# Kernel tuning notes

Measured on AMD Instinct MI355X. Metric: run time of the kernel, lower is better.

The kernel has to match this reference:

```python
import jax, jax.numpy as jnp
import numpy as np

B, H, S, D = 2, 16, 2048, 64


def setup_inputs() -> dict:
    key = jax.random.key(0)
    k1, k2, k3, k4 = jax.random.split(key, 4)
    Hin = jax.random.normal(k1, (B, H, S, D), dtype=jnp.float32)
    Hk = jax.random.normal(k2, (B, H, S, D), dtype=jnp.float32)
    Hv = jax.random.normal(k3, (B, H, S, D), dtype=jnp.float32)
    # causal lookahead mask: 1 above diagonal (disallowed), 0 elsewhere
    mask = jnp.triu(jnp.ones((S, S), dtype=jnp.float32), k=1)[None, None, :, :]
    # per-head learned G_LM cache matrix avAp: [H, D, D]
    avAp = jax.random.normal(k4, (H, D, D), dtype=jnp.float32) * (1.0 / np.sqrt(D))
    return {"Hin": Hin, "Hk": Hk, "Hv": Hv, "mask": mask, "avAp": avAp, "F_hidden": D}


def reference(Hin, Hk, Hv, mask, avAp, F_hidden):
    # WHiWHj = Hin @ avAp  : [B,H,S,D] x [H,D,D] -> [B,H,S,D]
    WHiWHj = jnp.einsum("bhsd,hde->bhse", Hin, avAp)
    # Ep = WHiWHj @ Hk^T / sqrt(dk) : [B,H,S,S]
    scale = 1.0 / jnp.sqrt(jnp.float32(F_hidden))
    Ep = jnp.einsum("bhse,bhte->bhst", WHiWHj, Hk) * scale
    E = jax.nn.softmax(Ep + mask * (-1e9), axis=-1)
    # Hout = E @ Hv : [B,H,S,D]
    return jnp.einsum("bhst,bhtd->bhsd", E, Hv)
```

## Files before the change

kernel.cpp:

```cpp
#include <hip/hip_runtime.h>

#define S_LEN 2048
#define NBH 32

typedef unsigned short u16;
typedef unsigned int u32;
typedef __attribute__((ext_vector_type(8))) short bf16x8;
typedef __attribute__((ext_vector_type(4))) float f32x4;

#define MFMA16(A, B, C) __builtin_amdgcn_mfma_f32_16x16x32_bf16(A, B, C, 0, 0, 0)

__device__ __forceinline__ u16 f2bf(float f) {
  u32 u = __builtin_bit_cast(u32, f);
  u += 0x7fffu + ((u >> 16) & 1u);
  return (u16)(u >> 16);
}
__device__ __forceinline__ float bf2f(u16 b) {
  u32 u = ((u32)b) << 16;
  return __builtin_bit_cast(float, u);
}
__device__ __forceinline__ u32 pack2(float a, float b) {
  return (u32)f2bf(a) | ((u32)f2bf(b) << 16);
}
__device__ __forceinline__ u32 cvtpk(float a, float b) {
  u32 r;
  asm("v_cvt_pk_bf16_f32 %0, %1, %2" : "=v"(r) : "v"(a), "v"(b));
  return r;
}
__device__ __forceinline__ void gld16(const void* g, void* l) {
  __builtin_amdgcn_global_load_lds(
      (const __attribute__((address_space(1))) void*)g,
      (__attribute__((address_space(3))) void*)l, 16, 0, 0);
}

__global__ __launch_bounds__(256) void prep_kernel(
    const float* __restrict__ Hk, const float* __restrict__ Hv,
    u16* __restrict__ Khb, u16* __restrict__ Klb, u16* __restrict__ Vtb) {
  __shared__ u16 sT[64 * 66];
  const int bh = blockIdx.y, t = blockIdx.x, tid = threadIdx.x;
  const size_t base = ((size_t)bh * S_LEN + t * 64) * 64;
  const size_t bb = ((size_t)bh * 32 + t) * 4096;

#pragma unroll
  for (int i = 0; i < 2; ++i) {
    int c = tid + 256 * i;
    int row = c >> 3, ci = c & 7;
    const float* ks = Hk + base + (size_t)row * 64 + ci * 8;
    float4 a = *(const float4*)ks, b = *(const float4*)(ks + 4);
    float xs[8] = {a.x, a.y, a.z, a.w, b.x, b.y, b.z, b.w};
    u16 hi[8], lo[8];
#pragma unroll
    for (int j = 0; j < 8; ++j) {
      hi[j] = f2bf(xs[j]);
      lo[j] = f2bf(xs[j] - bf2f(hi[j]));
    }
    int o = (c & ~7) | (ci ^ (row & 7));
    *(uint4*)(Khb + bb + o * 8) = *(uint4*)hi;
    *(uint4*)(Klb + bb + o * 8) = *(uint4*)lo;

    const float* vs = Hv + base + (size_t)row * 64 + ci * 8;
    float4 va = *(const float4*)vs, vb = *(const float4*)(vs + 4);
    u16* dst = sT + row * 66 + ci * 8;
    *(u32*)(dst + 0) = pack2(va.x, va.y);
    *(u32*)(dst + 2) = pack2(va.z, va.w);
    *(u32*)(dst + 4) = pack2(vb.x, vb.y);
    *(u32*)(dst + 6) = pack2(vb.z, vb.w);
  }
  __syncthreads();

#pragma unroll
  for (int i = 0; i < 2; ++i) {
    int o = tid + 256 * i;
    int d = o >> 3, s8 = ((o & 7) ^ (d & 7)) * 8;
    u16 tmp[8];
#pragma unroll
    for (int j = 0; j < 8; ++j) tmp[j] = sT[(s8 + j) * 66 + d];
    *(uint4*)(Vtb + bb + o * 8) = *(uint4*)tmp;
  }
}

__global__ __launch_bounds__(512, 4) void attn_kernel(
    const float* __restrict__ Hin, const float* __restrict__ avAp,
    const u16* __restrict__ Khb, const u16* __restrict__ Klb,
    const u16* __restrict__ Vtb, float* __restrict__ Out) {
  __shared__ __align__(16) char smem[65536];

  const int bh = blockIdx.y;
  const int h = bh & 15;
  const int x = blockIdx.x;
  const int qtile = ((bh >> 4) & 1) ? x : (15 - x);
  const int q0 = qtile * 128;
  const int tid = threadIdx.x, wave = tid >> 6, lane = tid & 63;
  const int lr = lane & 15, lg = lane >> 4;
  const int qrow = q0 + wave * 16 + lr;
  const int nT = 2 * qtile + 2;

#define STAGE(tt, bN)                                              \
  {                                                                \
    const size_t go = (((size_t)bh * 32 + (tt)) * 512 + tid) * 16; \
    char* lw = smem + (bN) + wave * 1024;                          \
    gld16((const char*)Khb + go, lw);                              \
    gld16((const char*)Klb + go, lw + 16384);                      \
    gld16((const char*)Vtb + go, lw + 32768);                      \
  }

  STAGE(0, 0);

  char* sAB = smem + 49152;
#pragma unroll
  for (int i = 0; i < 2; ++i) {
    int c = tid + 512 * i;
    int d = c >> 4, c4 = c & 15;
    int key = (((d >> 3) & 1) << 4) | (((d >> 4) & 1) << 6);
    *(float4*)(sAB + d * 256 + ((c4 * 16) ^ key)) =
        *(const float4*)(avAp + (size_t)h * 4096 + c * 4);
  }

  bf16x8 ahi[2], alo[2];
#pragma unroll
  for (int kk = 0; kk < 2; ++kk) {
    const float* src =
        Hin + ((size_t)bh * S_LEN + qrow) * 64 + kk * 32 + lg * 8;
    float4 u = *(const float4*)src;
    float4 w = *(const float4*)(src + 4);
    float xs[8] = {u.x, u.y, u.z, u.w, w.x, w.y, w.z, w.w};
#pragma unroll
    for (int j = 0; j < 8; ++j) {
      u16 hh = f2bf(xs[j]);
      ahi[kk][j] = (short)hh;
      alo[kk][j] = (short)f2bf(xs[j] - bf2f(hh));
    }
  }
  __syncthreads();

  const int keyA = ((lg & 1) << 4) | ((lg >> 1) << 6);
  f32x4 qa[4];
#pragma unroll
  for (int nb = 0; nb < 4; ++nb) qa[nb] = (f32x4){0.f, 0.f, 0.f, 0.f};
#pragma unroll
  for (int kk = 0; kk < 2; ++kk) {
    bf16x8 bhiK[4], bloK[4];
#pragma unroll
    for (int nb = 0; nb < 4; ++nb) {
#pragma unroll
      for (int j = 0; j < 8; ++j) {
        float xv = *(const float*)(sAB + (kk * 32 + lg * 8 + j) * 256 +
                                   (((nb * 16 + lr) * 4) ^ keyA));
        u16 hh = f2bf(xv);
        bhiK[nb][j] = (short)hh;
        bloK[nb][j] = (short)f2bf(xv - bf2f(hh));
      }
    }
#pragma unroll
    for (int nb = 0; nb < 4; ++nb) {
      qa[nb] = MFMA16(bhiK[nb], ahi[kk], qa[nb]);
      qa[nb] = MFMA16(bloK[nb], ahi[kk], qa[nb]);
      qa[nb] = MFMA16(bhiK[nb], alo[kk], qa[nb]);
    }
  }
  __syncthreads();

  const float QSCALE = 0.125f * 1.44269504088896f;
  char* sPw = smem + 49152 + wave * 2048;
  bf16x8 qhi[2], qlo[2];
#pragma unroll
  for (int nb = 0; nb < 4; ++nb) {
    uint2 w;
    w.x = pack2(qa[nb][0] * QSCALE, qa[nb][1] * QSCALE);
    w.y = pack2(qa[nb][2] * QSCALE, qa[nb][3] * QSCALE);
    *(uint2*)(sPw + lr * 128 + ((nb * 32 + lg * 8) ^ ((lr & 7) << 4))) = w;
  }
#pragma unroll
  for (int kk = 0; kk < 2; ++kk)
    qhi[kk] = *(const bf16x8*)(sPw + lr * 128 +
                               ((kk * 64 + lg * 16) ^ ((lr & 7) << 4)));
#pragma unroll
  for (int nb = 0; nb < 4; ++nb) {
    float v[4];
#pragma unroll
    for (int r = 0; r < 4; ++r) {
      float s = qa[nb][r] * QSCALE;
      v[r] = s - bf2f(f2bf(s));
    }
    uint2 w;
    w.x = pack2(v[0], v[1]);
    w.y = pack2(v[2], v[3]);
    *(uint2*)(sPw + lr * 128 + ((nb * 32 + lg * 8) ^ ((lr & 7) << 4))) = w;
  }
#pragma unroll
  for (int kk = 0; kk < 2; ++kk)
    qlo[kk] = *(const bf16x8*)(sPw + lr * 128 +
                               ((kk * 64 + lg * 16) ^ ((lr & 7) << 4)));

  f32x4 Oacc[4];
#pragma unroll
  for (int db = 0; db < 4; ++db) Oacc[db] = (f32x4){0.f, 0.f, 0.f, 0.f};
  float m_r = -3.0e38f, l_r = 0.f;
  int buf = 0;

  for (int t = 0; t < nT; ++t) {
    if (t + 1 < nT) STAGE(t + 1, (buf ^ 1) * 8192);
    const int bK = buf * 8192;
    const int kv0 = t * 64;

    if (kv0 <= q0 + wave * 16 + 15) {
      f32x4 sacc[4];
#pragma unroll
      for (int nb = 0; nb < 4; ++nb) sacc[nb] = (f32x4){0.f, 0.f, 0.f, 0.f};
#pragma unroll
      for (int nb = 0; nb < 4; ++nb) {
        int krow = nb * 16 + lr;
#pragma unroll
        for (int kk = 0; kk < 2; ++kk) {
          int off = krow * 128 + ((kk * 64 + lg * 16) ^ ((krow & 7) << 4));
          bf16x8 kh = *(const bf16x8*)(smem + bK + off);
          bf16x8 kl = *(const bf16x8*)(smem + 16384 + bK + off);
          sacc[nb] = MFMA16(kh, qhi[kk], sacc[nb]);
          sacc[nb] = MFMA16(kl, qhi[kk], sacc[nb]);
          sacc[nb] = MFMA16(kh, qlo[kk], sacc[nb]);
        }
      }

      if (kv0 + 63 > q0 + wave * 16) {
#pragma unroll
        for (int nb = 0; nb < 4; ++nb)
#pragma unroll
          for (int r = 0; r < 4; ++r)
            if (kv0 + nb * 16 + lg * 4 + r > qrow) sacc[nb][r] = -1.0e30f;
      }

      float tmax = sacc[0][0];
#pragma unroll
      for (int nb = 0; nb < 4; ++nb)
#pragma unroll
        for (int r = 0; r < 4; ++r) tmax = fmaxf(tmax, sacc[nb][r]);
      tmax = fmaxf(tmax, __shfl_xor(tmax, 16));
      tmax = fmaxf(tmax, __shfl_xor(tmax, 32));
      if (!__all(tmax <= m_r + 8.0f)) {
        float mn = fmaxf(m_r, tmax);
        float corr = exp2f(m_r - mn);
        m_r = mn;
        l_r *= corr;
#pragma unroll
        for (int db = 0; db < 4; ++db) Oacc[db] *= corr;
      }
      float rs = 0.f;
#pragma unroll
      for (int nb = 0; nb < 4; ++nb)
#pragma unroll
        for (int r = 0; r < 4; ++r) {
          float e = exp2f(sacc[nb][r] - m_r);
          sacc[nb][r] = e;
          rs += e;
        }
      rs += __shfl_xor(rs, 16);
      rs += __shfl_xor(rs, 32);
      l_r += rs;

#pragma unroll
      for (int nb = 0; nb < 4; ++nb) {
        uint2 w;
        w.x = cvtpk(sacc[nb][0], sacc[nb][1]);
        w.y = cvtpk(sacc[nb][2], sacc[nb][3]);
        *(uint2*)(sPw + lr * 128 + ((nb * 32 + lg * 8) ^ ((lr & 7) << 4))) = w;
      }
      bf16x8 pa[2];
#pragma unroll
      for (int kk = 0; kk < 2; ++kk)
        pa[kk] = *(const bf16x8*)(sPw + lr * 128 +
                                  ((kk * 64 + lg * 16) ^ ((lr & 7) << 4)));

#pragma unroll
      for (int db = 0; db < 4; ++db) {
        int vrow = db * 16 + lr;
#pragma unroll
        for (int kk = 0; kk < 2; ++kk) {
          int off = vrow * 128 + ((kk * 64 + lg * 16) ^ ((vrow & 7) << 4));
          bf16x8 vb = *(const bf16x8*)(smem + 32768 + bK + off);
          Oacc[db] = MFMA16(vb, pa[kk], Oacc[db]);
        }
      }
    }

    __syncthreads();
    buf ^= 1;
  }

  float invl = 1.0f / l_r;
  float* orow = Out + ((size_t)bh * S_LEN + qrow) * 64;
#pragma unroll
  for (int db = 0; db < 4; ++db) {
    float4 o = make_float4(Oacc[db][0] * invl, Oacc[db][1] * invl,
                           Oacc[db][2] * invl, Oacc[db][3] * invl);
    *(float4*)(orow + db * 16 + lg * 4) = o;
  }
#undef STAGE
}

extern "C" void kernel_launch(void* const* d_in, const int* in_sizes, int n_in,
                              void* d_out, int out_size, void* d_ws,
                              size_t ws_size, hipStream_t stream) {
  const float* Hin = (const float*)d_in[0];
  const float* Hk = (const float*)d_in[1];
  const float* Hv = (const float*)d_in[2];
  const float* avAp = (const float*)d_in[4];
  float* Out = (float*)d_out;

  const size_t N = (size_t)NBH * S_LEN * 64;
  u16* Khb = (u16*)d_ws;
  u16* Klb = Khb + N;
  u16* Vtb = Klb + N;

  prep_kernel<<<dim3(S_LEN / 64, NBH), dim3(256), 0, stream>>>(Hk, Hv, Khb,
                                                               Klb, Vtb);
  attn_kernel<<<dim3(S_LEN / 128, NBH), dim3(512), 0, stream>>>(
      Hin, avAp, Khb, Klb, Vtb, Out);
}
```

Before: 161.8 us.

## Switch to 32x32 MFMA with split-KV wave groups and in-register P repacking

Moves all matrix products from 16x16x32 to 32x32x16 bf16 MFMA. Each of the 8 waves now owns 32 query rows, and the two halves of the block process alternating KV tiles (split-K), with a final LDS-based merge of the softmax statistics and partial outputs. P and Q fragments are repacked in registers with permlane32_swap rather than round-tripping through LDS. The double-buffer prefetch overlap is replaced by staging a pair of tiles between two barriers, which trades the load/compute overlap for higher MFMA efficiency and fewer LDS transposes. It also adds the register cost of 16-wide accumulators.

```diff
diff --git a/kernel.cpp b/kernel.cpp
--- a/kernel.cpp
+++ b/kernel.cpp
@@ -6,9 +6,11 @@
 typedef unsigned short u16;
 typedef unsigned int u32;
 typedef __attribute__((ext_vector_type(8))) short bf16x8;
-typedef __attribute__((ext_vector_type(4))) float f32x4;
-
-#define MFMA16(A, B, C) __builtin_amdgcn_mfma_f32_16x16x32_bf16(A, B, C, 0, 0, 0)
+typedef __attribute__((ext_vector_type(16))) float f32x16;
+typedef __attribute__((ext_vector_type(2))) u32 u32x2;
+typedef __attribute__((ext_vector_type(4))) u32 u32x4;
+
+#define MFMA32(A, B, C) __builtin_amdgcn_mfma_f32_32x32x16_bf16(A, B, C, 0, 0, 0)
 
 __device__ __forceinline__ u16 f2bf(float f) {
   u32 u = __builtin_bit_cast(u32, f);
@@ -31,6 +33,22 @@
   __builtin_amdgcn_global_load_lds(
       (const __attribute__((address_space(1))) void*)g,
       (__attribute__((address_space(3))) void*)l, 16, 0, 0);
+}
+
+__device__ __forceinline__ void pack_bfrag(const f32x16& s, bf16x8& f0,
+                                           bf16x8& f1) {
+  u32 u0[4], u1[4];
+#pragma unroll
+  for (int m = 0; m < 4; ++m) {
+    u0[m] = cvtpk(s[4 * m], s[4 * m + 1]);
+    u1[m] = cvtpk(s[4 * m + 2], s[4 * m + 3]);
+  }
+  u32x2 a0 = __builtin_amdgcn_permlane32_swap(u0[0], u0[1], false, false);
+  u32x2 a1 = __builtin_amdgcn_permlane32_swap(u1[0], u1[1], false, false);
+  u32x2 a2 = __builtin_amdgcn_permlane32_swap(u0[2], u0[3], false, false);
+  u32x2 a3 = __builtin_amdgcn_permlane32_swap(u1[2], u1[3], false, false);
+  f0 = __builtin_bit_cast(bf16x8, (u32x4){a0.x, a1.x, a0.y, a1.y});
+  f1 = __builtin_bit_cast(bf16x8, (u32x4){a2.x, a3.x, a2.y, a3.y});
 }
 
 __global__ __launch_bounds__(256) void prep_kernel(
@@ -79,162 +97,152 @@
   }
 }
 
+__device__ __forceinline__ void stage_pair(char* smem, int bh, int p, int tid,
+                                           int wave, const u16* Khb,
+                                           const u16* Klb, const u16* Vtb) {
+#pragma unroll
+  for (int ts = 0; ts < 2; ++ts) {
+    const int tt = 2 * p + ts;
+    const size_t gb = (((size_t)bh * 32 + tt) * 512 + tid) * 16;
+    char* lb = smem + ts * 24576 + wave * 1024;
+    gld16((const char*)Khb + gb, lb);
+    gld16((const char*)Klb + gb, lb + 8192);
+    gld16((const char*)Vtb + gb, lb + 16384);
+  }
+}
+
 __global__ __launch_bounds__(512, 4) void attn_kernel(
     const float* __restrict__ Hin, const float* __restrict__ avAp,
     const u16* __restrict__ Khb, const u16* __restrict__ Klb,
     const u16* __restrict__ Vtb, float* __restrict__ Out) {
-  __shared__ __align__(16) char smem[65536];
+  __shared__ __align__(16) char smem[49152];
 
   const int bh = blockIdx.y;
-  const int h = bh & 15;
+  const int h16 = bh & 15;
   const int x = blockIdx.x;
   const int qtile = ((bh >> 4) & 1) ? x : (15 - x);
   const int q0 = qtile * 128;
   const int tid = threadIdx.x, wave = tid >> 6, lane = tid & 63;
-  const int lr = lane & 15, lg = lane >> 4;
-  const int qrow = q0 + wave * 16 + lr;
-  const int nT = 2 * qtile + 2;
-
-#define STAGE(tt, bN)                                              \
-  {                                                                \
-    const size_t go = (((size_t)bh * 32 + (tt)) * 512 + tid) * 16; \
-    char* lw = smem + (bN) + wave * 1024;                          \
-    gld16((const char*)Khb + go, lw);                              \
-    gld16((const char*)Klb + go, lw + 16384);                      \
-    gld16((const char*)Vtb + go, lw + 32768);                      \
-  }
-
-  STAGE(0, 0);
-
-  char* sAB = smem + 49152;
+  const int ql = lane & 31;
+  const int hh = lane >> 5;
+  const int wq = wave & 3;
+  const int kset = wave >> 2;
+  const int qrow = q0 + wq * 32 + ql;
+  const int npair = qtile + 1;
+
+  float* sAf = (float*)smem;
 #pragma unroll
   for (int i = 0; i < 2; ++i) {
     int c = tid + 512 * i;
-    int d = c >> 4, c4 = c & 15;
-    int key = (((d >> 3) & 1) << 4) | (((d >> 4) & 1) << 6);
-    *(float4*)(sAB + d * 256 + ((c4 * 16) ^ key)) =
-        *(const float4*)(avAp + (size_t)h * 4096 + c * 4);
-  }
-
-  bf16x8 ahi[2], alo[2];
-#pragma unroll
-  for (int kk = 0; kk < 2; ++kk) {
+    *(float4*)(sAf + c * 4) =
+        *(const float4*)(avAp + (size_t)h16 * 4096 + c * 4);
+  }
+
+  bf16x8 bhin_hi[4], bhin_lo[4];
+#pragma unroll
+  for (int ks = 0; ks < 4; ++ks) {
     const float* src =
-        Hin + ((size_t)bh * S_LEN + qrow) * 64 + kk * 32 + lg * 8;
+        Hin + ((size_t)bh * S_LEN + qrow) * 64 + ks * 16 + hh * 8;
     float4 u = *(const float4*)src;
     float4 w = *(const float4*)(src + 4);
     float xs[8] = {u.x, u.y, u.z, u.w, w.x, w.y, w.z, w.w};
 #pragma unroll
     for (int j = 0; j < 8; ++j) {
-      u16 hh = f2bf(xs[j]);
-      ahi[kk][j] = (short)hh;
-      alo[kk][j] = (short)f2bf(xs[j] - bf2f(hh));
-    }
-  }
-  __syncthreads();
-
-  const int keyA = ((lg & 1) << 4) | ((lg >> 1) << 6);
-  f32x4 qa[4];
-#pragma unroll
-  for (int nb = 0; nb < 4; ++nb) qa[nb] = (f32x4){0.f, 0.f, 0.f, 0.f};
-#pragma unroll
-  for (int kk = 0; kk < 2; ++kk) {
-    bf16x8 bhiK[4], bloK[4];
-#pragma unroll
-    for (int nb = 0; nb < 4; ++nb) {
+      u16 t = f2bf(xs[j]);
+      bhin_hi[ks][j] = (short)t;
+      bhin_lo[ks][j] = (short)f2bf(xs[j] - bf2f(t));
+    }
+  }
+  __syncthreads();
+
+  f32x16 qacc[2];
+  qacc[0] = (f32x16)0.0f;
+  qacc[1] = (f32x16)0.0f;
+#pragma unroll
+  for (int ks = 0; ks < 4; ++ks) {
+#pragma unroll
+    for (int nb = 0; nb < 2; ++nb) {
+      bf16x8 ahi, alo;
 #pragma unroll
       for (int j = 0; j < 8; ++j) {
-        float xv = *(const float*)(sAB + (kk * 32 + lg * 8 + j) * 256 +
-                                   (((nb * 16 + lr) * 4) ^ keyA));
-        u16 hh = f2bf(xv);
-        bhiK[nb][j] = (short)hh;
-        bloK[nb][j] = (short)f2bf(xv - bf2f(hh));
-      }
-    }
-#pragma unroll
-    for (int nb = 0; nb < 4; ++nb) {
-      qa[nb] = MFMA16(bhiK[nb], ahi[kk], qa[nb]);
-      qa[nb] = MFMA16(bloK[nb], ahi[kk], qa[nb]);
-      qa[nb] = MFMA16(bhiK[nb], alo[kk], qa[nb]);
-    }
-  }
-  __syncthreads();
+        float v = sAf[(ks * 16 + hh * 8 + j) * 64 + nb * 32 + ql];
+        u16 t = f2bf(v);
+        ahi[j] = (short)t;
+        alo[j] = (short)f2bf(v - bf2f(t));
+      }
+      qacc[nb] = MFMA32(ahi, bhin_hi[ks], qacc[nb]);
+      qacc[nb] = MFMA32(alo, bhin_hi[ks], qacc[nb]);
+      qacc[nb] = MFMA32(ahi, bhin_lo[ks], qacc[nb]);
+    }
+  }
+  __syncthreads();
+
+  stage_pair(smem, bh, 0, tid, wave, Khb, Klb, Vtb);
 
   const float QSCALE = 0.125f * 1.44269504088896f;
-  char* sPw = smem + 49152 + wave * 2048;
-  bf16x8 qhi[2], qlo[2];
-#pragma unroll
-  for (int nb = 0; nb < 4; ++nb) {
-    uint2 w;
-    w.x = pack2(qa[nb][0] * QSCALE, qa[nb][1] * QSCALE);
-    w.y = pack2(qa[nb][2] * QSCALE, qa[nb][3] * QSCALE);
-    *(uint2*)(sPw + lr * 128 + ((nb * 32 + lg * 8) ^ ((lr & 7) << 4))) = w;
-  }
-#pragma unroll
-  for (int kk = 0; kk < 2; ++kk)
-    qhi[kk] = *(const bf16x8*)(sPw + lr * 128 +
-                               ((kk * 64 + lg * 16) ^ ((lr & 7) << 4)));
-#pragma unroll
-  for (int nb = 0; nb < 4; ++nb) {
-    float v[4];
-#pragma unroll
-    for (int r = 0; r < 4; ++r) {
-      float s = qa[nb][r] * QSCALE;
-      v[r] = s - bf2f(f2bf(s));
-    }
-    uint2 w;
-    w.x = pack2(v[0], v[1]);
-    w.y = pack2(v[2], v[3]);
-    *(uint2*)(sPw + lr * 128 + ((nb * 32 + lg * 8) ^ ((lr & 7) << 4))) = w;
-  }
-#pragma unroll
-  for (int kk = 0; kk < 2; ++kk)
-    qlo[kk] = *(const bf16x8*)(sPw + lr * 128 +
-                               ((kk * 64 + lg * 16) ^ ((lr & 7) << 4)));
-
-  f32x4 Oacc[4];
-#pragma unroll
-  for (int db = 0; db < 4; ++db) Oacc[db] = (f32x4){0.f, 0.f, 0.f, 0.f};
+  bf16x8 qhi[4], qlo[4];
+#pragma unroll
+  for (int nb = 0; nb < 2; ++nb) {
+    f32x16 s, lo;
+#pragma unroll
+    for (int r = 0; r < 16; ++r) {
+      float v = qacc[nb][r] * QSCALE;
+      s[r] = v;
+      lo[r] = v - bf2f(f2bf(v));
+    }
+    pack_bfrag(s, qhi[nb * 2], qhi[nb * 2 + 1]);
+    pack_bfrag(lo, qlo[nb * 2], qlo[nb * 2 + 1]);
+  }
+
+  f32x16 Oacc[2];
+  Oacc[0] = (f32x16)0.0f;
+  Oacc[1] = (f32x16)0.0f;
   float m_r = -3.0e38f, l_r = 0.f;
-  int buf = 0;
-
-  for (int t = 0; t < nT; ++t) {
-    if (t + 1 < nT) STAGE(t + 1, (buf ^ 1) * 8192);
-    const int bK = buf * 8192;
+
+  __syncthreads();
+
+  for (int p = 0; p < npair; ++p) {
+    const int t = 2 * p + kset;
     const int kv0 = t * 64;
-
-    if (kv0 <= q0 + wave * 16 + 15) {
-      f32x4 sacc[4];
-#pragma unroll
-      for (int nb = 0; nb < 4; ++nb) sacc[nb] = (f32x4){0.f, 0.f, 0.f, 0.f};
-#pragma unroll
-      for (int nb = 0; nb < 4; ++nb) {
-        int krow = nb * 16 + lr;
-#pragma unroll
-        for (int kk = 0; kk < 2; ++kk) {
-          int off = krow * 128 + ((kk * 64 + lg * 16) ^ ((krow & 7) << 4));
-          bf16x8 kh = *(const bf16x8*)(smem + bK + off);
-          bf16x8 kl = *(const bf16x8*)(smem + 16384 + bK + off);
-          sacc[nb] = MFMA16(kh, qhi[kk], sacc[nb]);
-          sacc[nb] = MFMA16(kl, qhi[kk], sacc[nb]);
-          sacc[nb] = MFMA16(kh, qlo[kk], sacc[nb]);
+    const char* base = smem + kset * 24576;
+
+    if (kv0 <= q0 + wq * 32 + 31) {
+      f32x16 sacc[2];
+      sacc[0] = (f32x16)0.0f;
+      sacc[1] = (f32x16)0.0f;
+#pragma unroll
+      for (int nb = 0; nb < 2; ++nb) {
+        const int krow = nb * 32 + ql;
+        const int swz = (krow & 7) << 4;
+#pragma unroll
+        for (int ks = 0; ks < 4; ++ks) {
+          const int off = krow * 128 + (((ks * 2 + hh) * 16) ^ swz);
+          bf16x8 kh = *(const bf16x8*)(base + off);
+          bf16x8 kl = *(const bf16x8*)(base + 8192 + off);
+          sacc[nb] = MFMA32(kh, qhi[ks], sacc[nb]);
+          sacc[nb] = MFMA32(kl, qhi[ks], sacc[nb]);
+          sacc[nb] = MFMA32(kh, qlo[ks], sacc[nb]);
         }
       }
 
-      if (kv0 + 63 > q0 + wave * 16) {
-#pragma unroll
-        for (int nb = 0; nb < 4; ++nb)
-#pragma unroll
-          for (int r = 0; r < 4; ++r)
-            if (kv0 + nb * 16 + lg * 4 + r > qrow) sacc[nb][r] = -1.0e30f;
-      }
-
-      float tmax = sacc[0][0];
-#pragma unroll
-      for (int nb = 0; nb < 4; ++nb)
-#pragma unroll
-        for (int r = 0; r < 4; ++r) tmax = fmaxf(tmax, sacc[nb][r]);
-      tmax = fmaxf(tmax, __shfl_xor(tmax, 16));
+      if (kv0 + 63 > q0 + wq * 32) {
+#pragma unroll
+        for (int nb = 0; nb < 2; ++nb)
+#pragma unroll
+          for (int r = 0; r < 16; ++r) {
+            int kv = kv0 + nb * 32 + (r & 3) + 8 * (r >> 2) + 4 * hh;
+            if (kv > qrow) sacc[nb][r] = -1.0e30f;
+          }
+      }
+
+      float a[16];
+#pragma unroll
+      for (int i = 0; i < 16; ++i) a[i] = fmaxf(sacc[0][i], sacc[1][i]);
+#pragma unroll
+      for (int i = 0; i < 8; ++i) a[i] = fmaxf(a[i], a[i + 8]);
+#pragma unroll
+      for (int i = 0; i < 4; ++i) a[i] = fmaxf(a[i], a[i + 4]);
+      float tmax = fmaxf(fmaxf(a[0], a[1]), fmaxf(a[2], a[3]));
       tmax = fmaxf(tmax, __shfl_xor(tmax, 32));
       if (!__all(tmax <= m_r + 8.0f)) {
         float mn = fmaxf(m_r, tmax);
@@ -242,59 +250,80 @@
         m_r = mn;
         l_r *= corr;
 #pragma unroll
-        for (int db = 0; db < 4; ++db) Oacc[db] *= corr;
-      }
-      float rs = 0.f;
-#pragma unroll
-      for (int nb = 0; nb < 4; ++nb)
-#pragma unroll
-        for (int r = 0; r < 4; ++r) {
-          float e = exp2f(sacc[nb][r] - m_r);
-          sacc[nb][r] = e;
-          rs += e;
-        }
-      rs += __shfl_xor(rs, 16);
+        for (int db = 0; db < 2; ++db)
+#pragma unroll
+          for (int r = 0; r < 16; ++r) Oacc[db][r] *= corr;
+      }
+#pragma unroll
+      for (int nb = 0; nb < 2; ++nb)
+#pragma unroll
+        for (int r = 0; r < 16; ++r) sacc[nb][r] = exp2f(sacc[nb][r] - m_r);
+#pragma unroll
+      for (int i = 0; i < 16; ++i) a[i] = sacc[0][i] + sacc[1][i];
+#pragma unroll
+      for (int i = 0; i < 8; ++i) a[i] += a[i + 8];
+#pragma unroll
+      for (int i = 0; i < 4; ++i) a[i] += a[i + 4];
+      float rs = (a[0] + a[1]) + (a[2] + a[3]);
       rs += __shfl_xor(rs, 32);
       l_r += rs;
 
-#pragma unroll
-      for (int nb = 0; nb < 4; ++nb) {
-        uint2 w;
-        w.x = cvtpk(sacc[nb][0], sacc[nb][1]);
-        w.y = cvtpk(sacc[nb][2], sacc[nb][3]);
-        *(uint2*)(sPw + lr * 128 + ((nb * 32 + lg * 8) ^ ((lr & 7) << 4))) = w;
-      }
-      bf16x8 pa[2];
-#pragma unroll
-      for (int kk = 0; kk < 2; ++kk)
-        pa[kk] = *(const bf16x8*)(sPw + lr * 128 +
-                                  ((kk * 64 + lg * 16) ^ ((lr & 7) << 4)));
-
-#pragma unroll
-      for (int db = 0; db < 4; ++db) {
-        int vrow = db * 16 + lr;
-#pragma unroll
-        for (int kk = 0; kk < 2; ++kk) {
-          int off = vrow * 128 + ((kk * 64 + lg * 16) ^ ((vrow & 7) << 4));
-          bf16x8 vb = *(const bf16x8*)(smem + 32768 + bK + off);
-          Oacc[db] = MFMA16(vb, pa[kk], Oacc[db]);
+      bf16x8 pa[4];
+      pack_bfrag(sacc[0], pa[0], pa[1]);
+      pack_bfrag(sacc[1], pa[2], pa[3]);
+
+#pragma unroll
+      for (int db = 0; db < 2; ++db) {
+        const int vrow = db * 32 + ql;
+        const int swz = (vrow & 7) << 4;
+#pragma unroll
+        for (int ks = 0; ks < 4; ++ks) {
+          const int off = vrow * 128 + (((ks * 2 + hh) * 16) ^ swz);
+          bf16x8 vb = *(const bf16x8*)(base + 16384 + off);
+          Oacc[db] = MFMA32(vb, pa[ks], Oacc[db]);
         }
       }
     }
 
     __syncthreads();
-    buf ^= 1;
-  }
-
-  float invl = 1.0f / l_r;
-  float* orow = Out + ((size_t)bh * S_LEN + qrow) * 64;
-#pragma unroll
-  for (int db = 0; db < 4; ++db) {
-    float4 o = make_float4(Oacc[db][0] * invl, Oacc[db][1] * invl,
-                           Oacc[db][2] * invl, Oacc[db][3] * invl);
-    *(float4*)(orow + db * 16 + lg * 4) = o;
-  }
-#undef STAGE
+    if (p + 1 < npair) stage_pair(smem, bh, p + 1, tid, wave, Khb, Klb, Vtb);
+    __syncthreads();
+  }
+
+  const int idx = wq * 64 + lane;
+  if (kset == 1) {
+#pragma unroll
+    for (int db = 0; db < 2; ++db)
+#pragma unroll
+      for (int m4 = 0; m4 < 4; ++m4) {
+        float4 v = make_float4(Oacc[db][4 * m4], Oacc[db][4 * m4 + 1],
+                               Oacc[db][4 * m4 + 2], Oacc[db][4 * m4 + 3]);
+        *(float4*)(smem + idx * 144 + db * 64 + m4 * 16) = v;
+      }
+    *(float*)(smem + 36864 + idx * 8) = m_r;
+    *(float*)(smem + 36864 + idx * 8 + 4) = l_r;
+  }
+  __syncthreads();
+  if (kset == 0) {
+    float mp = *(const float*)(smem + 36864 + idx * 8);
+    float lp = *(const float*)(smem + 36864 + idx * 8 + 4);
+    float mo = fmaxf(m_r, mp);
+    float ca = exp2f(m_r - mo), cb = exp2f(mp - mo);
+    float linv = 1.0f / (l_r * ca + lp * cb);
+    float* orow = Out + ((size_t)bh * S_LEN + qrow) * 64;
+#pragma unroll
+    for (int db = 0; db < 2; ++db)
+#pragma unroll
+      for (int m4 = 0; m4 < 4; ++m4) {
+        float4 vp = *(const float4*)(smem + idx * 144 + db * 64 + m4 * 16);
+        float4 o;
+        o.x = (Oacc[db][4 * m4 + 0] * ca + vp.x * cb) * linv;
+        o.y = (Oacc[db][4 * m4 + 1] * ca + vp.y * cb) * linv;
+        o.z = (Oacc[db][4 * m4 + 2] * ca + vp.z * cb) * linv;
+        o.w = (Oacc[db][4 * m4 + 3] * ca + vp.w * cb) * linv;
+        *(float4*)(orow + db * 32 + m4 * 8 + hh * 4) = o;
+      }
+  }
 }
 
 extern "C" void kernel_launch(void* const* d_in, const int* in_sizes, int n_in,
```

Result: slower. 171.7 us (+6.2%).
